# Optimization experiments

Measured on AMD Instinct MI355X. Metric: run time of the kernel, lower is better.

The kernel has to match this reference:

```python
import jax, jax.numpy as jnp
import numpy as np
from jax import lax

DIM = 256
NUM_HEADS = 8
SW = 7
HEAD_DIM = DIM // NUM_HEADS
SCALE = HEAD_DIM ** -0.5


def setup_inputs() -> dict:
    key = jax.random.key(0)
    ks = jax.random.split(key, 7)
    B, C, H, W = 8, DIM, 56, 56
    x = jax.random.normal(ks[0], (B, C, H, W), dtype=jnp.float32)
    w_qkv = jax.random.normal(ks[1], (3 * C, C), dtype=jnp.float32) * 0.02
    b_qkv = jnp.zeros((3 * C,), dtype=jnp.float32)
    # depthwise 3x3 kernel, OIHW with feature_group_count=C -> (C,1,3,3)
    w_dw = jax.random.normal(ks[2], (C, 1, 3, 3), dtype=jnp.float32) * 0.02
    b_dw = jnp.zeros((C,), dtype=jnp.float32)
    w_proj = jax.random.normal(ks[3], (C, C), dtype=jnp.float32) * 0.02
    b_proj = jnp.zeros((C,), dtype=jnp.float32)
    return {"x": x, "w_qkv": w_qkv, "b_qkv": b_qkv, "w_dw": w_dw,
            "b_dw": b_dw, "w_proj": w_proj, "b_proj": b_proj}


def _conv1x1(x, w, b):
    # x:[B,C,H,W], w:[O,C] -> [B,O,H,W]
    return jnp.einsum('bchw,oc->bohw', x, w) + b[None, :, None, None]


def _dwconv3x3(x, w, b):
    C = x.shape[1]
    y = lax.conv_general_dilated(x, w, window_strides=(1, 1), padding='SAME',
                                 dimension_numbers=('NCHW', 'OIHW', 'NCHW'),
                                 feature_group_count=C)
    return y + b[None, :, None, None]


def _stripe_attn_H(q, k, v, sw):
    # q,k,v: [B,h,C,H,W]; local attention within sw-thick horizontal stripes
    B, h, C, H, W = q.shape
    sw = min(sw, H)
    pad = (-H) % sw
    if pad:
        pw = [(0, 0)] * 3 + [(0, pad), (0, 0)]
        q = jnp.pad(q, pw); k = jnp.pad(k, pw); v = jnp.pad(v, pw)
    Hp = H + pad
    n = Hp // sw

    def rs(t):
        # -> [B,h,n, sw*W, C]
        return t.reshape(B, h, C, n, sw, W).transpose(0, 1, 3, 4, 5, 2).reshape(B, h, n, sw * W, C)

    qs, ks_, vs = rs(q) * SCALE, rs(k), rs(v)
    attn = jax.nn.softmax(jnp.einsum('bhnqc,bhnkc->bhnqk', qs, ks_), axis=-1)
    out = jnp.einsum('bhnqk,bhnkc->bhnqc', attn, vs)
    out = out.reshape(B, h, n, sw, W, C).transpose(0, 1, 5, 2, 3, 4).reshape(B, h, C, Hp, W)
    return out[:, :, :, :H, :]


def _stripe_attn_W(q, k, v, sw):
    # attention within sw-thick vertical stripes; softmax is permutation-
    # equivariant over the stripe sequence, so transposing H<->W and reusing
    # the H-stripe kernel computes identical math.
    t = lambda a: a.transpose(0, 1, 2, 4, 3)
    return t(_stripe_attn_H(t(q), t(k), t(v), sw))


def reference(x, w_qkv, b_qkv, w_dw, b_dw, w_proj, b_proj):
    B, C, H, W = x.shape
    hh = NUM_HEADS // 2
    qkv = _conv1x1(x, w_qkv, b_qkv)
    q, k, v = jnp.split(qkv, 3, axis=1)
    v = v + _dwconv3x3(v, w_dw, b_dw)

    def heads(t):
        return t.reshape(B, NUM_HEADS, HEAD_DIM, H, W)

    q, k, v = heads(q), heads(k), heads(v)
    out_h = _stripe_attn_H(q[:, :hh], k[:, :hh], v[:, :hh], SW)
    out_w = _stripe_attn_W(q[:, hh:], k[:, hh:], v[:, hh:], SW)
    out = jnp.concatenate([out_h, out_w], axis=1).reshape(B, C, H, W)
    return _conv1x1(out, w_proj, b_proj)
```

## Files before the change

### kernel.cpp

```cpp
#include <hip/hip_runtime.h>
#include <hip/hip_bf16.h>
#include <stdint.h>

#define Bn 8
#define Cn 256
#define Hn 56
#define Wn 56
#define HWn 3136
#define NHEADS 8
#define HDIM 32
#define SEQ 392
#define NSTR 8
#define QKV_LD 768
#define KSC (0.17677669529663689f * 1.4426950408889634f)

#if __has_builtin(__builtin_amdgcn_exp2f)
#define EXP2(x) __builtin_amdgcn_exp2f(x)
#else
#define EXP2(x) exp2f(x)
#endif

typedef short short8 __attribute__((ext_vector_type(8)));
typedef float floatx4 __attribute__((ext_vector_type(4)));

__device__ __forceinline__ unsigned short f2bf(float f) {
  union { float f; uint32_t u; } v; v.f = f;
  uint32_t u = v.u;
  u += 0x7fffu + ((u >> 16) & 1u);
  return (unsigned short)(u >> 16);
}
__device__ __forceinline__ float bf2f(unsigned short h) {
  union { uint32_t u; float f; } v; v.u = ((uint32_t)h) << 16;
  return v.f;
}
__device__ __forceinline__ uint32_t cvt_pk_bf16(float lo, float hi) {
  uint32_t r;
  asm("v_cvt_pk_bf16_f32 %0, %1, %2" : "=v"(r) : "v"(lo), "v"(hi));
  return r;
}
__device__ __forceinline__ void gload16(const unsigned short* g, unsigned short* l) {
  __builtin_amdgcn_global_load_lds((const __attribute__((address_space(1))) void*)g,
                                   (__attribute__((address_space(3))) void*)l, 16, 0, 0);
}

__global__ __launch_bounds__(256) void k_prep(const float* __restrict__ wa,
                                              const float* __restrict__ wb,
                                              unsigned short* __restrict__ da,
                                              unsigned short* __restrict__ db,
                                              const float* __restrict__ x,
                                              unsigned short* __restrict__ xt) {
  int bx = blockIdx.x;
  int t = threadIdx.x;
  if (bx < 256) {
    int i = bx * 256 + t;
    if (i < 49152) {
      float4 v = ((const float4*)wa)[i];
      ushort4 o;
      o.x = f2bf(v.x); o.y = f2bf(v.y); o.z = f2bf(v.z); o.w = f2bf(v.w);
      ((ushort4*)da)[i] = o;
    } else {
      int k = i - 49152;
      float4 v = ((const float4*)wb)[k];
      ushort4 o;
      o.x = f2bf(v.x); o.y = f2bf(v.y); o.z = f2bf(v.z); o.w = f2bf(v.w);
      ((ushort4*)db)[k] = o;
    }
    return;
  }
  __shared__ float tile[32][33];
  int tx = bx - 256;
  int pb = tx % 98, cb = (tx / 98) & 7, b = tx / 784;
  int c = t >> 3, p4 = (t & 7) * 4;
  float4 v = *(const float4*)(x + (((size_t)b * Cn + cb * 32 + c) * HWn + pb * 32 + p4));
  tile[c][p4 + 0] = v.x; tile[c][p4 + 1] = v.y; tile[c][p4 + 2] = v.z; tile[c][p4 + 3] = v.w;
  __syncthreads();
  int p = t >> 3, c4 = (t & 7) * 4;
  ushort4 o;
  o.x = f2bf(tile[c4 + 0][p]); o.y = f2bf(tile[c4 + 1][p]);
  o.z = f2bf(tile[c4 + 2][p]); o.w = f2bf(tile[c4 + 3][p]);
  *(ushort4*)(xt + (((size_t)b * HWn + pb * 32 + p) * Cn + cb * 32 + c4)) = o;
}

__global__ __launch_bounds__(512) void k_gemm0(const unsigned short* __restrict__ A,
                                               const unsigned short* __restrict__ Bt,
                                               const float* __restrict__ bias,
                                               unsigned short* __restrict__ qkh,
                                               unsigned short* __restrict__ outV) {
  const int K = 256, N = HWn;
  __shared__ __align__(16) unsigned short SH[16384];
  unsigned short* As = SH;
  unsigned short* Bs = SH + 8192;
  int t = threadIdx.x;
  int raw = blockIdx.x;
  int chunk = gridDim.x >> 3;
  int wg = (raw & 7) * chunk + (raw >> 3);
  int b = wg / 150, r = wg % 150;
  int m0 = (r % 6) * 128, n0 = (r / 6) * 128;
  const unsigned short* Bb = Bt + (size_t)b * N * K;
  int lane = t & 63, w = t >> 6;
  int wr = w >> 1, wc = w & 1;
  int g = lane >> 4, q = lane & 15;
  int rt = t >> 2, st = t & 3;
  int cs = st ^ (rt & 3);
  const unsigned short* Ag = A + (size_t)(m0 + rt) * K + cs * 8;
  int nr = n0 + rt;
  const unsigned short* Bg = Bb + (size_t)((nr < N) ? nr : (N - 1)) * K + cs * 8;
  int ldst = t * 8;

  floatx4 z4 = {0.f, 0.f, 0.f, 0.f};
  floatx4 acc[2][4];
#pragma unroll
  for (int i = 0; i < 2; i++)
#pragma unroll
    for (int j = 0; j < 4; j++) acc[i][j] = z4;

#define STAGE0(kt, off) do {                                                   \
    gload16(Ag + (kt) * 32, &As[(off) + ldst]);                                \
    gload16(Bg + (kt) * 32, &Bs[(off) + ldst]);                                \
  } while (0)

#define COMPUTE0(off) do {                                                     \
    short8 af[2], bfr[4];                                                      \
    _Pragma("unroll")                                                          \
    for (int i = 0; i < 2; i++) {                                              \
      int row = wr * 32 + i * 16 + q;                                          \
      af[i] = *(const short8*)&As[(off) + row * 32 + ((g ^ (q & 3)) << 3)];    \
    }                                                                          \
    _Pragma("unroll")                                                          \
    for (int j = 0; j < 4; j++) {                                              \
      int row = wc * 64 + j * 16 + q;                                          \
      bfr[j] = *(const short8*)&Bs[(off) + row * 32 + ((g ^ (q & 3)) << 3)];   \
    }                                                                          \
    _Pragma("unroll")                                                          \
    for (int i = 0; i < 2; i++)                                                \
      _Pragma("unroll")                                                        \
      for (int j = 0; j < 4; j++)                                              \
        acc[i][j] = __builtin_amdgcn_mfma_f32_16x16x32_bf16(af[i], bfr[j], acc[i][j], 0, 0, 0); \
  } while (0)

  STAGE0(0, 0);
  STAGE0(1, 4096);
#pragma unroll
  for (int tt = 0; tt < 8; tt++) {
    if (tt < 7) { asm volatile("s_waitcnt vmcnt(2)" ::: "memory"); }
    else       { asm volatile("s_waitcnt vmcnt(0)" ::: "memory"); }
    __syncthreads();
    COMPUTE0((tt & 1) * 4096);
    __syncthreads();
    if (tt < 6) STAGE0(tt + 2, (tt & 1) * 4096);
  }
#undef STAGE0
#undef COMPUTE0

  unsigned short* E = SH;
#pragma unroll
  for (int i = 0; i < 2; i++) {
    int ob = m0 + wr * 32 + i * 16 + g * 4;
    float bs0 = bias[ob + 0], bs1 = bias[ob + 1], bs2 = bias[ob + 2], bs3 = bias[ob + 3];
    float sc = (ob >= 256 && ob < 512) ? KSC : 1.0f;
    int lobg = wr * 4 + i * 2 + (g >> 1);
#pragma unroll
    for (int j = 0; j < 4; j++) {
      int lc = wc * 64 + j * 16 + q;
      ushort4 o;
      o.x = f2bf((acc[i][j][0] + bs0) * sc);
      o.y = f2bf((acc[i][j][1] + bs1) * sc);
      o.z = f2bf((acc[i][j][2] + bs2) * sc);
      o.w = f2bf((acc[i][j][3] + bs3) * sc);
      *(ushort4*)&E[lc * 128 + ((lobg ^ (lc & 7)) << 3) + (g & 1) * 4] = o;
    }
  }
  __syncthreads();
  int c = t >> 2, part = t & 3;
  int col = n0 + c;
  if (col < N) {
    int mt = m0 >> 7;
    unsigned short* dst;
    if (mt < 4) {
      int hd = (mt & 1) * 4 + part;
      int sl = (mt >> 1) * 8 + hd;
      int p_ord = (hd >= 4) ? ((col % Wn) * Wn + col / Wn) : col;
      dst = qkh + (((size_t)b * 16 + sl) * HWn + p_ord) * 32;
    } else {
      dst = outV + ((size_t)b * HWn + col) * 256 + (m0 - 512) + part * 32;
    }
#pragma unroll
    for (int k2 = part * 4; k2 < part * 4 + 4; k2++) {
      short8 v = *(const short8*)&E[c * 128 + ((k2 ^ (c & 7)) << 3)];
      *(short8*)(dst + (k2 - part * 4) * 8) = v;
    }
  }
}

__global__ __launch_bounds__(512) void k_gemm1(const unsigned short* __restrict__ A,
                                               const unsigned short* __restrict__ Bt,
                                               const float* __restrict__ bias,
                                               float* __restrict__ outF,
                                               int M, int N, int nm, int nper) {
  const int K = 256;
  __shared__ __align__(16) char SH[67584];
  unsigned short* As = (unsigned short*)SH;
  unsigned short* Bs = As + 16384;
  int t = threadIdx.x;
  int raw = blockIdx.x;
  int chunk = gridDim.x >> 3;
  int wg = (raw & 7) * chunk + (raw >> 3);
  int b = wg / nper, r = wg % nper;
  int m0 = (r % nm) * 128, n0 = (r / nm) * 128;
  const unsigned short* Bb = Bt + (size_t)b * N * K;
  int lane = t & 63, w = t >> 6;
  int wr = w >> 1, wc = w & 1;
  int g = lane >> 4, q = lane & 15;
  int srow8 = lane >> 3;
  int slot = lane & 7;

  const unsigned short* Ag[2];
  const unsigned short* Bg[2];
  int ldst[2];
#pragma unroll
  for (int i = 0; i < 2; i++) {
    int row = i * 64 + w * 8 + srow8;
    int cs = slot ^ srow8;
    Ag[i] = A + (size_t)(m0 + row) * K + cs * 8;
    int nr = n0 + row;
    Bg[i] = Bb + (size_t)((nr < N) ? nr : (N - 1)) * K + cs * 8;
    ldst[i] = (i * 64 + w * 8) * 64;
  }

  floatx4 z4 = {0.f, 0.f, 0.f, 0.f};
  floatx4 acc[2][4];
#pragma unroll
  for (int i = 0; i < 2; i++)
#pragma unroll
    for (int j = 0; j < 4; j++) acc[i][j] = z4;

#define STAGE(kt, off) do {                                                    \
    _Pragma("unroll")                                                          \
    for (int i = 0; i < 2; i++) gload16(Ag[i] + (kt) * 64, &As[(off) + ldst[i]]); \
    _Pragma("unroll")                                                          \
    for (int i = 0; i < 2; i++) gload16(Bg[i] + (kt) * 64, &Bs[(off) + ldst[i]]); \
  } while (0)

#define COMPUTE(off) do {                                                      \
    _Pragma("unroll")                                                          \
    for (int kk = 0; kk < 64; kk += 32) {                                      \
      short8 af[2], bfr[4];                                                    \
      _Pragma("unroll")                                                        \
      for (int i = 0; i < 2; i++) {                                            \
        int row = wr * 32 + i * 16 + q;                                        \
        af[i] = *(const short8*)&As[(off) + row * 64 + ((((kk >> 3) + g) ^ (q & 7)) << 3)]; \
      }                                                                        \
      _Pragma("unroll")                                                        \
      for (int j = 0; j < 4; j++) {                                            \
        int row = wc * 64 + j * 16 + q;                                        \
        bfr[j] = *(const short8*)&Bs[(off) + row * 64 + ((((kk >> 3) + g) ^ (q & 7)) << 3)]; \
      }                                                                        \
      _Pragma("unroll")                                                        \
      for (int i = 0; i < 2; i++)                                              \
        _Pragma("unroll")                                                      \
        for (int j = 0; j < 4; j++)                                            \
          acc[i][j] = __builtin_amdgcn_mfma_f32_16x16x32_bf16(af[i], bfr[j], acc[i][j], 0, 0, 0); \
    }                                                                          \
  } while (0)

  STAGE(0, 0);
  STAGE(1, 8192);
  asm volatile("s_waitcnt vmcnt(4)" ::: "memory");
  __syncthreads();
  COMPUTE(0);
  __syncthreads();
  STAGE(2, 0);
  asm volatile("s_waitcnt vmcnt(4)" ::: "memory");
  __syncthreads();
  COMPUTE(8192);
  __syncthreads();
  STAGE(3, 8192);
  asm volatile("s_waitcnt vmcnt(4)" ::: "memory");
  __syncthreads();
  COMPUTE(0);
  asm volatile("s_waitcnt vmcnt(0)" ::: "memory");
  __syncthreads();
  COMPUTE(8192);
#undef STAGE
#undef COMPUTE

  __syncthreads();
  float* Ef = (float*)SH;
#pragma unroll
  for (int i = 0; i < 2; i++) {
    int ob = m0 + wr * 32 + i * 16 + g * 4;
    int lob = wr * 32 + i * 16 + g * 4;
    float bs0 = bias[ob + 0], bs1 = bias[ob + 1], bs2 = bias[ob + 2], bs3 = bias[ob + 3];
#pragma unroll
    for (int j = 0; j < 4; j++) {
      int lc = wc * 64 + j * 16 + q;
      Ef[(lob + 0) * 132 + lc] = acc[i][j][0] + bs0;
      Ef[(lob + 1) * 132 + lc] = acc[i][j][1] + bs1;
      Ef[(lob + 2) * 132 + lc] = acc[i][j][2] + bs2;
      Ef[(lob + 3) * 132 + lc] = acc[i][j][3] + bs3;
    }
  }
  __syncthreads();
  int rr = t >> 2, seg = t & 3;
  float* dst = outF + (size_t)b * M * N + (size_t)(m0 + rr) * N + n0;
#pragma unroll
  for (int k2 = 0; k2 < 8; k2++) {
    int col = seg * 32 + k2 * 4;
    if (n0 + col < N) {
      floatx4 v = *(const floatx4*)&Ef[rr * 132 + col];
      *(floatx4*)(dst + col) = v;
    }
  }
}

__global__ __launch_bounds__(512) void k_dwconv_t(const unsigned short* __restrict__ vb,
                                                  const float* __restrict__ wdw,
                                                  const float* __restrict__ bdw,
                                                  unsigned short* __restrict__ vmt) {
  __shared__ float wS[1152];
  __shared__ float bS[128];
  __shared__ __align__(16) unsigned short tile[32][140];
  int t = threadIdx.x;
  int pass = blockIdx.y, b = blockIdx.z;
  for (int i = t; i < 1152; i += 512) wS[i] = wdw[pass * 1152 + i];
  if (t < 128) bS[t] = bdw[pass * 128 + t];
  __syncthreads();

  int pi = t >> 4, c8 = (t & 15) * 8;
  int i32 = blockIdx.x * 32 + pi;
  int h, w;
  if (pass == 0) { h = i32 / Wn; w = i32 % Wn; }
  else           { w = i32 / Hn; h = i32 % Hn; }

  const unsigned short* vq = vb + pass * 128 + c8;
  float a[8];
  short8 vc = *(const short8*)(vq + ((size_t)b * HWn + h * Wn + w) * 256);
#pragma unroll
  for (int e = 0; e < 8; e++) a[e] = bf2f((unsigned short)vc[e]) + bS[c8 + e];
#pragma unroll
  for (int ky = 0; ky < 3; ky++) {
    int hh = h + ky - 1;
    if (hh < 0 || hh >= Hn) continue;
#pragma unroll
    for (int kx = 0; kx < 3; kx++) {
      int ww = w + kx - 1;
      if (ww < 0 || ww >= Wn) continue;
      short8 vn = *(const short8*)(vq + ((size_t)b * HWn + hh * Wn + ww) * 256);
#pragma unroll
      for (int e = 0; e < 8; e++) a[e] += bf2f((unsigned short)vn[e]) * wS[(c8 + e) * 9 + ky * 3 + kx];
    }
  }
  short8 o;
#pragma unroll
  for (int e = 0; e < 8; e++) o[e] = (short)f2bf(a[e]);
  *(short8*)&tile[pi][c8] = o;
  __syncthreads();

  int dd = t >> 2, quarter = t & 3;
  short8 ov;
#pragma unroll
  for (int k2 = 0; k2 < 8; k2++) ov[k2] = (short)tile[quarter * 8 + k2][dd];
  *(short8*)(vmt + ((size_t)(b * Cn + pass * 128 + dd)) * HWn + blockIdx.x * 32 + quarter * 8) = ov;
}

__global__ __launch_bounds__(512) void k_attn(const unsigned short* __restrict__ qkh,
                                              const unsigned short* __restrict__ vmt,
                                              unsigned short* __restrict__ aout) {
  __shared__ __align__(16) unsigned short Ks[12288];
  __shared__ __align__(16) unsigned short Vf[12800];
  __shared__ __align__(16) unsigned short Pf[4096];
  int s = blockIdx.x;
  int hd = blockIdx.y & 7, b = blockIdx.y >> 3;
  int t = threadIdx.x, lane = t & 63, wv = t >> 6;
  bool wst = (hd >= 4);
  int q = lane & 15, g = lane >> 4;
  int sbase = s * SEQ;

  const unsigned short* qh = qkh + (((size_t)b * 16 + hd) * HWn + sbase) * 32;
  const unsigned short* kh = qkh + (((size_t)b * 16 + 8 + hd) * HWn + sbase) * 32;

  short8 qpre[4];
#pragma unroll
  for (int it = 0; it < 4; it++) {
    int qb = it * 8 + wv;
    int qi = qb * 16 + q;
    int qil = (qi < SEQ) ? qi : 391;
    qpre[it] = *(const short8*)(qh + (size_t)qil * 32 + g * 8);
  }

#pragma unroll
  for (int P = 0; P < 3; P++) {
    int key = P * 128 + (t >> 2);
    int gg = t & 3;
    short8 kv = *(const short8*)(kh + (size_t)key * 32 + gg * 8);
    *(short8*)&Ks[((((key >> 4) * 4 + gg) * 16) + (key & 15)) * 8] = kv;
  }
  short8 kf24;
  {
    int key = 384 + q; if (key > 391) key = 391;
    kf24 = *(const short8*)(kh + (size_t)key * 32 + g * 8);
  }
  const unsigned short* vg = vmt + ((size_t)(b * Cn + hd * HDIM)) * HWn + sbase;
  for (int idx = t; idx < 1600; idx += 512) {
    int d = idx / 50, Gc = idx % 50;
    short8 vv = *(const short8*)(vg + (size_t)d * HWn + Gc * 8);
    *(short8*)&Vf[(Gc * 32 + (d ^ (Gc & 7))) * 8] = vv;
  }
  __syncthreads();

  floatx4 z4 = {0.f, 0.f, 0.f, 0.f};
  unsigned short* Pw = &Pf[wv * 512];
  int gh = g >> 1, ge = (g & 1) * 4;

#pragma unroll
  for (int it = 0; it < 4; it++) {
    int qb = it * 8 + wv;
    if (qb >= 25) continue;
    int qi = qb * 16 + q;
    int qil = (qi < SEQ) ? qi : 391;
    short8 qf = qpre[it];

    floatx4 sph[13];
    float sm = 0.f;
    floatx4 o0 = z4, o1 = z4;

#define WRITEPX(sA_, sB_, validB) do {                                         \
    uint2 wA, wB;                                                              \
    wA.x = cvt_pk_bf16((sA_)[0], (sA_)[1]);                                    \
    wA.y = cvt_pk_bf16((sA_)[2], (sA_)[3]);                                    \
    if (validB) {                                                              \
      wB.x = cvt_pk_bf16((sB_)[0], (sB_)[1]);                                  \
      wB.y = cvt_pk_bf16((sB_)[2], (sB_)[3]);                                  \
    } else { wB.x = 0u; wB.y = 0u; }                                           \
    *(uint2*)&Pw[(gh * 16 + q) * 8 + ge] = wA;                                 \
    *(uint2*)&Pw[((2 + gh) * 16 + q) * 8 + ge] = wB;                           \
  } while (0)

#define PVSTEP(ch) do {                                                        \
    asm volatile("s_waitcnt lgkmcnt(0)" ::: "memory");                         \
    short8 pfr = *(const short8*)&Pw[(g * 16 + q) * 8];                        \
    int Gc = (ch) * 4 + g; if (Gc > 49) Gc = 49;                               \
    int sw = Gc & 7;                                                           \
    short8 vf0 = *(const short8*)&Vf[(Gc * 32 + (q ^ sw)) * 8];                \
    short8 vf1 = *(const short8*)&Vf[(Gc * 32 + 16 + (q ^ sw)) * 8];           \
    pfr_ = pfr; vf0_ = vf0; vf1_ = vf1;                                        \
  } while (0)

    short8 pfr_, vf0_, vf1_;

    __builtin_amdgcn_s_setprio(1);
#pragma unroll
    for (int j = 0; j < 12; j++) {
      short8 kf = *(const short8*)&Ks[((j * 4 + g) * 16 + q) * 8];
      sph[j] = __builtin_amdgcn_mfma_f32_16x16x32_bf16(kf, qf, z4, 0, 0, 0);
    }
    __builtin_amdgcn_s_setprio(0);
#pragma unroll
    for (int j = 0; j < 12; j++) {
      float e0 = EXP2(sph[j][0]); float e1 = EXP2(sph[j][1]);
      float e2 = EXP2(sph[j][2]); float e3 = EXP2(sph[j][3]);
      sph[j][0] = e0; sph[j][1] = e1; sph[j][2] = e2; sph[j][3] = e3;
      sm += (e0 + e1) + (e2 + e3);
    }
    WRITEPX(sph[0], sph[1], true);
#pragma unroll
    for (int ch = 0; ch < 6; ch++) {
      PVSTEP(ch);
      if (ch < 5) {
        switch (ch + 1) {
          case 1: WRITEPX(sph[2], sph[3], true); break;
          case 2: WRITEPX(sph[4], sph[5], true); break;
          case 3: WRITEPX(sph[6], sph[7], true); break;
          case 4: WRITEPX(sph[8], sph[9], true); break;
          case 5: WRITEPX(sph[10], sph[11], true); break;
        }
      }
      __builtin_amdgcn_s_setprio(1);
      o0 = __builtin_amdgcn_mfma_f32_16x16x32_bf16(vf0_, pfr_, o0, 0, 0, 0);
      o1 = __builtin_amdgcn_mfma_f32_16x16x32_bf16(vf1_, pfr_, o1, 0, 0, 0);
      __builtin_amdgcn_s_setprio(0);
    }

    __builtin_amdgcn_s_setprio(1);
#pragma unroll
    for (int j = 0; j < 12; j++) {
      short8 kf = *(const short8*)&Ks[(((j + 12) * 4 + g) * 16 + q) * 8];
      sph[j] = __builtin_amdgcn_mfma_f32_16x16x32_bf16(kf, qf, z4, 0, 0, 0);
    }
    sph[12] = __builtin_amdgcn_mfma_f32_16x16x32_bf16(kf24, qf, z4, 0, 0, 0);
    __builtin_amdgcn_s_setprio(0);
    if (g >= 2) { sph[12][0] = sph[12][1] = sph[12][2] = sph[12][3] = -3.0e38f; }
#pragma unroll
    for (int j = 0; j < 13; j++) {
      float e0 = EXP2(sph[j][0]); float e1 = EXP2(sph[j][1]);
      float e2 = EXP2(sph[j][2]); float e3 = EXP2(sph[j][3]);
      sph[j][0] = e0; sph[j][1] = e1; sph[j][2] = e2; sph[j][3] = e3;
      sm += (e0 + e1) + (e2 + e3);
    }
    WRITEPX(sph[0], sph[1], true);
#pragma unroll
    for (int ch = 6; ch < 13; ch++) {
      PVSTEP(ch);
      if (ch < 12) {
        switch (ch + 1) {
          case 7:  WRITEPX(sph[2], sph[3], true); break;
          case 8:  WRITEPX(sph[4], sph[5], true); break;
          case 9:  WRITEPX(sph[6], sph[7], true); break;
          case 10: WRITEPX(sph[8], sph[9], true); break;
          case 11: WRITEPX(sph[10], sph[11], true); break;
          case 12: WRITEPX(sph[12], sph[12], false); break;
        }
      }
      __builtin_amdgcn_s_setprio(1);
      o0 = __builtin_amdgcn_mfma_f32_16x16x32_bf16(vf0_, pfr_, o0, 0, 0, 0);
      o1 = __builtin_amdgcn_mfma_f32_16x16x32_bf16(vf1_, pfr_, o1, 0, 0, 0);
      __builtin_amdgcn_s_setprio(0);
    }
#undef WRITEPX
#undef PVSTEP

    sm += __shfl_xor(sm, 16);
    sm += __shfl_xor(sm, 32);
    float rcp = 1.0f / sm;

    if (qi < SEQ) {
      int pq = wst ? ((qil % Wn) * Wn + s * 7 + qil / Wn) : (sbase + qil);
      size_t ob = ((size_t)b * HWn + pq) * Cn + hd * HDIM;
      ushort4 u0, u1;
      u0.x = f2bf(o0[0] * rcp); u0.y = f2bf(o0[1] * rcp);
      u0.z = f2bf(o0[2] * rcp); u0.w = f2bf(o0[3] * rcp);
      u1.x = f2bf(o1[0] * rcp); u1.y = f2bf(o1[1] * rcp);
      u1.z = f2bf(o1[2] * rcp); u1.w = f2bf(o1[3] * rcp);
      *(ushort4*)(aout + ob + g * 4) = u0;
      *(ushort4*)(aout + ob + 16 + g * 4) = u1;
    }
  }
}

extern "C" void kernel_launch(void* const* d_in, const int* in_sizes, int n_in,
                              void* d_out, int out_size, void* d_ws, size_t ws_size,
                              hipStream_t stream) {
  const float* x     = (const float*)d_in[0];
  const float* wqkv  = (const float*)d_in[1];
  const float* bqkv  = (const float*)d_in[2];
  const float* wdw   = (const float*)d_in[3];
  const float* bdw   = (const float*)d_in[4];
  const float* wproj = (const float*)d_in[5];
  const float* bproj = (const float*)d_in[6];
  float* out = (float*)d_out;

  unsigned short* xt   = (unsigned short*)d_ws;
  unsigned short* wqb  = xt + (size_t)Bn * HWn * Cn;
  unsigned short* wpb  = wqb + 768 * 256;
  unsigned short* qkh  = wpb + 256 * 256;
  unsigned short* vb   = qkh + (size_t)Bn * 16 * HWn * 32;
  unsigned short* vmt  = vb + (size_t)Bn * HWn * Cn;
  unsigned short* aout = vmt + (size_t)Bn * HWn * Cn;

  k_prep<<<dim3(256 + 98 * 8 * Bn), 256, 0, stream>>>(wqkv, wproj, wqb, wpb, x, xt);
  k_gemm0<<<dim3(1200), 512, 0, stream>>>(wqb, xt, bqkv, qkh, vb);
  k_dwconv_t<<<dim3(98, 2, Bn), 512, 0, stream>>>(vb, wdw, bdw, vmt);
  k_attn<<<dim3(NSTR, Bn * NHEADS), 512, 0, stream>>>(qkh, vmt, aout);
  k_gemm1<<<dim3(400), 512, 0, stream>>>(wpb, aout, bproj, out, 256, HWn, 2, 50);
}
```

Baseline: 102.4 us.

## Fuse depthwise 3x3 conv of V into the stripe attention kernel

```diff
diff --git a/kernel.cpp b/kernel.cpp
--- a/kernel.cpp
+++ b/kernel.cpp
@@ -313,71 +313,31 @@
   }
 }
 
-__global__ __launch_bounds__(512) void k_dwconv_t(const unsigned short* __restrict__ vb,
-                                                  const float* __restrict__ wdw,
-                                                  const float* __restrict__ bdw,
-                                                  unsigned short* __restrict__ vmt) {
-  __shared__ float wS[1152];
-  __shared__ float bS[128];
-  __shared__ __align__(16) unsigned short tile[32][140];
-  int t = threadIdx.x;
-  int pass = blockIdx.y, b = blockIdx.z;
-  for (int i = t; i < 1152; i += 512) wS[i] = wdw[pass * 1152 + i];
-  if (t < 128) bS[t] = bdw[pass * 128 + t];
-  __syncthreads();
-
-  int pi = t >> 4, c8 = (t & 15) * 8;
-  int i32 = blockIdx.x * 32 + pi;
-  int h, w;
-  if (pass == 0) { h = i32 / Wn; w = i32 % Wn; }
-  else           { w = i32 / Hn; h = i32 % Hn; }
-
-  const unsigned short* vq = vb + pass * 128 + c8;
-  float a[8];
-  short8 vc = *(const short8*)(vq + ((size_t)b * HWn + h * Wn + w) * 256);
-#pragma unroll
-  for (int e = 0; e < 8; e++) a[e] = bf2f((unsigned short)vc[e]) + bS[c8 + e];
-#pragma unroll
-  for (int ky = 0; ky < 3; ky++) {
-    int hh = h + ky - 1;
-    if (hh < 0 || hh >= Hn) continue;
-#pragma unroll
-    for (int kx = 0; kx < 3; kx++) {
-      int ww = w + kx - 1;
-      if (ww < 0 || ww >= Wn) continue;
-      short8 vn = *(const short8*)(vq + ((size_t)b * HWn + hh * Wn + ww) * 256);
-#pragma unroll
-      for (int e = 0; e < 8; e++) a[e] += bf2f((unsigned short)vn[e]) * wS[(c8 + e) * 9 + ky * 3 + kx];
-    }
-  }
-  short8 o;
-#pragma unroll
-  for (int e = 0; e < 8; e++) o[e] = (short)f2bf(a[e]);
-  *(short8*)&tile[pi][c8] = o;
-  __syncthreads();
-
-  int dd = t >> 2, quarter = t & 3;
-  short8 ov;
-#pragma unroll
-  for (int k2 = 0; k2 < 8; k2++) ov[k2] = (short)tile[quarter * 8 + k2][dd];
-  *(short8*)(vmt + ((size_t)(b * Cn + pass * 128 + dd)) * HWn + blockIdx.x * 32 + quarter * 8) = ov;
-}
-
 __global__ __launch_bounds__(512) void k_attn(const unsigned short* __restrict__ qkh,
-                                              const unsigned short* __restrict__ vmt,
+                                              const unsigned short* __restrict__ vb,
+                                              const float* __restrict__ wdw,
+                                              const float* __restrict__ bdw,
                                               unsigned short* __restrict__ aout) {
   __shared__ __align__(16) unsigned short Ks[12288];
   __shared__ __align__(16) unsigned short Vf[12800];
   __shared__ __align__(16) unsigned short Pf[4096];
+  __shared__ __align__(16) unsigned short tileV[128 * 42];
+  __shared__ float wS[288];
+  __shared__ float bS[32];
   int s = blockIdx.x;
   int hd = blockIdx.y & 7, b = blockIdx.y >> 3;
   int t = threadIdx.x, lane = t & 63, wv = t >> 6;
   bool wst = (hd >= 4);
   int q = lane & 15, g = lane >> 4;
   int sbase = s * SEQ;
+  int c0 = hd * 32;
 
   const unsigned short* qh = qkh + (((size_t)b * 16 + hd) * HWn + sbase) * 32;
   const unsigned short* kh = qkh + (((size_t)b * 16 + 8 + hd) * HWn + sbase) * 32;
+  const unsigned short* vbb = vb + (size_t)b * HWn * 256 + c0;
+
+  if (t < 288) wS[t] = wdw[(c0 + t / 9) * 9 + t % 9];
+  if (t >= 288 && t < 320) bS[t - 288] = bdw[c0 + t - 288];
 
   short8 qpre[4];
 #pragma unroll
@@ -400,13 +360,58 @@
     int key = 384 + q; if (key > 391) key = 391;
     kf24 = *(const short8*)(kh + (size_t)key * 32 + g * 8);
   }
-  const unsigned short* vg = vmt + ((size_t)(b * Cn + hd * HDIM)) * HWn + sbase;
-  for (int idx = t; idx < 1600; idx += 512) {
-    int d = idx / 50, Gc = idx % 50;
-    short8 vv = *(const short8*)(vg + (size_t)d * HWn + Gc * 8);
-    *(short8*)&Vf[(Gc * 32 + (d ^ (Gc & 7))) * 8] = vv;
-  }
-  __syncthreads();
+  __syncthreads();
+
+  {
+    int pi = t >> 4, cp = (t & 15) * 2;
+    int Gcl = t & 15, d = t >> 4;
+#pragma unroll
+    for (int pass = 0; pass < 4; pass++) {
+#pragma unroll
+      for (int jj = 0; jj < 4; jj++) {
+        int row = jj * 32 + pi;
+        int i = pass * 128 + row;
+        float a0 = 0.f, a1 = 0.f;
+        if (i < SEQ) {
+          int hp, wp;
+          if (wst) { hp = i % 56; wp = s * 7 + i / 56; }
+          else     { hp = s * 7 + i / 56; wp = i % 56; }
+          a0 = bS[cp]; a1 = bS[cp + 1];
+          uint32_t cc = *(const uint32_t*)(vbb + (size_t)(hp * 56 + wp) * 256 + cp);
+          a0 += bf2f((unsigned short)(cc & 0xffff));
+          a1 += bf2f((unsigned short)(cc >> 16));
+#pragma unroll
+          for (int dy = 0; dy < 3; dy++) {
+            int hh = hp + dy - 1;
+            if (hh < 0 || hh >= Hn) continue;
+#pragma unroll
+            for (int dx = 0; dx < 3; dx++) {
+              int ww = wp + dx - 1;
+              if (ww < 0 || ww >= Wn) continue;
+              uint32_t vv = *(const uint32_t*)(vbb + (size_t)(hh * 56 + ww) * 256 + cp);
+              a0 += bf2f((unsigned short)(vv & 0xffff)) * wS[cp * 9 + dy * 3 + dx];
+              a1 += bf2f((unsigned short)(vv >> 16)) * wS[(cp + 1) * 9 + dy * 3 + dx];
+            }
+          }
+        }
+        int dsw = cp ^ ((row & 7) << 2);
+        ushort2 o; o.x = f2bf(a0); o.y = f2bf(a1);
+        *(ushort2*)&tileV[row * 42 + dsw] = o;
+      }
+      __syncthreads();
+      int Gc = pass * 16 + Gcl;
+      if (Gc < 50) {
+        short8 gr;
+#pragma unroll
+        for (int e = 0; e < 8; e++) {
+          int row = Gcl * 8 + e;
+          gr[e] = (short)tileV[row * 42 + (d ^ ((row & 7) << 2))];
+        }
+        *(short8*)&Vf[(Gc * 32 + (d ^ (Gc & 7))) * 8] = gr;
+      }
+      __syncthreads();
+    }
+  }
 
   floatx4 z4 = {0.f, 0.f, 0.f, 0.f};
   unsigned short* Pw = &Pf[wv * 512];
@@ -554,12 +559,10 @@
   unsigned short* wpb  = wqb + 768 * 256;
   unsigned short* qkh  = wpb + 256 * 256;
   unsigned short* vb   = qkh + (size_t)Bn * 16 * HWn * 32;
-  unsigned short* vmt  = vb + (size_t)Bn * HWn * Cn;
-  unsigned short* aout = vmt + (size_t)Bn * HWn * Cn;
+  unsigned short* aout = vb + (size_t)Bn * HWn * Cn;
 
   k_prep<<<dim3(256 + 98 * 8 * Bn), 256, 0, stream>>>(wqkv, wproj, wqb, wpb, x, xt);
   k_gemm0<<<dim3(1200), 512, 0, stream>>>(wqb, xt, bqkv, qkh, vb);
-  k_dwconv_t<<<dim3(98, 2, Bn), 512, 0, stream>>>(vb, wdw, bdw, vmt);
-  k_attn<<<dim3(NSTR, Bn * NHEADS), 512, 0, stream>>>(qkh, vmt, aout);
+  k_attn<<<dim3(NSTR, Bn * NHEADS), 512, 0, stream>>>(qkh, vb, wdw, bdw, aout);
   k_gemm1<<<dim3(400), 512, 0, stream>>>(wpb, aout, bproj, out, 256, HWn, 2, 50);
 }
```

After: 111.8 us. 1.09x slower.
